# Performance work log

Hardware: AMD Instinct MI355X
Metric: run time of the kernel (lower is better)

## Reference

```python
import jax, jax.numpy as jnp
import numpy as np

BN_EPS = 1e-5


def maxpool2(x):
    # 2x2 max pool, stride 2: (B,C,H,W) -> (B,C,H//2,W//2)
    B, C, H, W = x.shape
    return x.reshape(B, C, H // 2, 2, W // 2, 2).max(axis=(3, 5))


def setup_inputs() -> dict:
    key = jax.random.key(0)
    ks = jax.random.split(key, 6)
    B, C, H, W = 4, 64, 96, 96   # in_dim = 64
    K, OD = 64, 64               # key_dim, out_dim
    sc = lambda fan: 1.0 / np.sqrt(fan)
    return {
        "c2": jax.random.normal(ks[0], (B, C, H, W), jnp.float32),
        "x": jax.random.normal(ks[1], (B, C, H, W), jnp.float32),
        # edge_att: Conv2d(2C->OD, 1x1, no bias) -> BN -> ReLU -> Conv2d(OD->1, 1x1) -> Sigmoid
        "w_ea1": jax.random.normal(ks[2], (OD, 2 * C), jnp.float32) * sc(2 * C),
        "bn_w": jnp.ones((OD,), jnp.float32),
        "bn_b": jnp.zeros((OD,), jnp.float32),
        "bn_m": jnp.zeros((OD,), jnp.float32),
        "bn_v": jnp.ones((OD,), jnp.float32),
        "w_ea2": jax.random.normal(ks[3], (1, OD), jnp.float32) * sc(OD),
        "b_ea2": jnp.zeros((1,), jnp.float32),
        # query_conv (shared for query AND key in the original forward)
        "w_q": jax.random.normal(ks[4], (K, C), jnp.float32) * sc(C),
        "b_q": jnp.zeros((K,), jnp.float32),
        "gamma": jnp.full((1,), 0.5, jnp.float32),
    }


def reference(c2, x, w_ea1, bn_w, bn_b, bn_m, bn_v, w_ea2, b_ea2, w_q, b_q, gamma):
    xp = maxpool2(x)        # (B,C,Hp,Wp)
    c2p = maxpool2(c2)
    B, C, H, W = x.shape
    Hp, Wp = xp.shape[2], xp.shape[3]

    # edge attention gate on pooled features -> (B,1,Hp,Wp)
    cat = jnp.concatenate([c2p, xp], axis=1)                       # (B,2C,Hp,Wp)
    h = jnp.einsum('oc,bchw->bohw', w_ea1, cat)
    bn_scale = (bn_w / jnp.sqrt(bn_v + BN_EPS))[None, :, None, None]
    h = jax.nn.relu((h - bn_m[None, :, None, None]) * bn_scale + bn_b[None, :, None, None])
    ea = jax.nn.sigmoid(jnp.einsum('oc,bchw->bohw', w_ea2, h) + b_ea2[None, :, None, None])

    # query at full res, key at pooled res (SAME conv weights, as in the source)
    q = jnp.einsum('kc,bchw->bkhw', w_q, x) + b_q[None, :, None, None]    # (B,K,H,W)
    k = jnp.einsum('kc,bchw->bkhw', w_q, xp) + b_q[None, :, None, None]   # (B,K,Hp,Wp)

    pq = q.reshape(B, -1, H * W)        # (B,K,N)
    pk = k.reshape(B, -1, Hp * Wp)      # (B,K,M)
    energy = jnp.einsum('bkn,bkm->bnm', pq, pk)                    # (B,N,M)
    attn = jax.nn.softmax(energy * ea.reshape(B, 1, Hp * Wp), axis=-1)

    v = xp.reshape(B, C, Hp * Wp)                                   # (B,C,M)
    out = jnp.einsum('bcm,bnm->bcn', v, attn).reshape(B, C, H, W)
    return gamma[0] * out + x
```

## Files before the change

kernel.cpp:

```cpp
#include <hip/hip_runtime.h>
#include <stdint.h>

#define B_ 4
#define C_ 64
#define H_ 96
#define W_ 96
#define HP_ 48
#define WP_ 48
#define N_ (H_*W_)
#define M_ (HP_*WP_)
#define KD_ 64
#define OD_ 64
#define BN_EPS 1e-5f
#define LOG2E 1.4426950408889634f
#define SHIFT2 28.853900817779268f
#define QT_ 48
#define QI_ (QT_/16)
#define QB_ (N_/QT_)
#define KVB_ 128
#define NT2_ (M_/KVB_)
#define KBUF_ 16384
#define BUF_ 32768
#define EAOFF_ 65536

typedef __bf16 bf16_t;
typedef bf16_t bf16x8 __attribute__((ext_vector_type(8)));
typedef bf16_t bf16x4 __attribute__((ext_vector_type(4)));
typedef float f32x4 __attribute__((ext_vector_type(4)));
typedef short short4v __attribute__((ext_vector_type(4)));
typedef short short8v __attribute__((ext_vector_type(8)));

static __device__ __forceinline__ unsigned short f2bf(float f) {
    unsigned int u = __builtin_bit_cast(unsigned int, f);
    u += 0x7fffu + ((u >> 16) & 1u);
    return (unsigned short)(u >> 16);
}

static __device__ __forceinline__ void gl_lds16(const unsigned short* g, unsigned short* l) {
#if __has_builtin(__builtin_amdgcn_global_load_lds)
    __builtin_amdgcn_global_load_lds(
        (const __attribute__((address_space(1))) unsigned int*)(const void*)g,
        (__attribute__((address_space(3))) unsigned int*)(void*)l, 16, 0, 0);
#endif
}

static __device__ __forceinline__ void setprio1() {
#if __has_builtin(__builtin_amdgcn_s_setprio)
    __builtin_amdgcn_s_setprio(1);
#endif
}
static __device__ __forceinline__ void setprio0() {
#if __has_builtin(__builtin_amdgcn_s_setprio)
    __builtin_amdgcn_s_setprio(0);
#endif
}
static __device__ __forceinline__ void schedbar0() {
#if __has_builtin(__builtin_amdgcn_sched_barrier)
    __builtin_amdgcn_sched_barrier(0);
#endif
}
static __device__ __forceinline__ void rawbar() {
#if __has_builtin(__builtin_amdgcn_s_barrier)
    __builtin_amdgcn_s_barrier();
#else
    __syncthreads();
#endif
}

__global__ __launch_bounds__(256) void prep_kernel(
    const float* __restrict__ x, const float* __restrict__ c2,
    const float* __restrict__ wq, const float* __restrict__ bq,
    const float* __restrict__ w1, const float* __restrict__ bnw, const float* __restrict__ bnb,
    const float* __restrict__ bnm, const float* __restrict__ bnv,
    const float* __restrict__ w2, const float* __restrict__ b2,
    unsigned short* __restrict__ kb, unsigned short* __restrict__ vb, float* __restrict__ ea) {

    __shared__ float lw1[OD_*2*C_];
    __shared__ float lwq[KD_*C_];
    __shared__ float xs[C_*33];
    __shared__ float c2s[C_*33];
    __shared__ float red[8][32];

    int tid = threadIdx.x;
    int b = blockIdx.x / 72;
    int m0 = (blockIdx.x % 72) * 32;

    for (int i = tid; i < OD_*2*C_; i += 256) lw1[i] = w1[i];
    for (int i = tid; i < KD_*C_; i += 256) lwq[i] = wq[i];
    for (int j = tid; j < 2048; j += 256) {
        int c = j >> 5, p = j & 31;
        int m = m0 + p;
        int hp = m / WP_, wp = m % WP_;
        size_t base = ((size_t)(b*C_ + c)*H_ + 2*hp)*W_ + 2*wp;
        const float* px = x + base;
        float mx = fmaxf(fmaxf(px[0], px[1]), fmaxf(px[W_], px[W_+1]));
        xs[c*33 + p] = mx;
        vb[(size_t)(b*C_ + c)*M_ + m] = f2bf(mx);
        const float* pc = c2 + base;
        c2s[c*33 + p] = fmaxf(fmaxf(pc[0], pc[1]), fmaxf(pc[W_], pc[W_+1]));
    }
    __syncthreads();

    int ml = tid & 31, oz = tid >> 5;
    int m = m0 + ml;

    float h[8] = {0,0,0,0,0,0,0,0};
    for (int c = 0; c < C_; c += 4) {
        float x0 = xs[c*33+ml], x1 = xs[(c+1)*33+ml], x2 = xs[(c+2)*33+ml], x3 = xs[(c+3)*33+ml];
        #pragma unroll
        for (int oi = 0; oi < 8; oi++) {
            const float4 wv = *(const float4*)&lwq[(oz*8 + oi)*C_ + c];
            h[oi] = fmaf(wv.x, x0, fmaf(wv.y, x1, fmaf(wv.z, x2, fmaf(wv.w, x3, h[oi]))));
        }
    }
    unsigned short tmp[8];
    #pragma unroll
    for (int oi = 0; oi < 8; oi++) tmp[oi] = f2bf(h[oi] + bq[oz*8 + oi]);
    *(uint4*)&kb[((size_t)b*M_ + m)*KD_ + oz*8] = *(const uint4*)tmp;

    float g[8] = {0,0,0,0,0,0,0,0};
    for (int c = 0; c < 2*C_; c += 4) {
        const float* srcb = (c < C_) ? &c2s[c*33] : &xs[(c - C_)*33];
        float x0 = srcb[ml], x1 = srcb[33+ml], x2 = srcb[66+ml], x3 = srcb[99+ml];
        #pragma unroll
        for (int oi = 0; oi < 8; oi++) {
            const float4 wv = *(const float4*)&lw1[(oz*8 + oi)*(2*C_) + c];
            g[oi] = fmaf(wv.x, x0, fmaf(wv.y, x1, fmaf(wv.z, x2, fmaf(wv.w, x3, g[oi]))));
        }
    }
    float z = 0.f;
    #pragma unroll
    for (int oi = 0; oi < 8; oi++) {
        int o = oz*8 + oi;
        float sc = bnw[o] * rsqrtf(bnv[o] + BN_EPS);
        float t = (g[oi] - bnm[o]) * sc + bnb[o];
        z += w2[o] * fmaxf(t, 0.f);
    }
    red[oz][ml] = z;
    __syncthreads();
    if (oz == 0) {
        float s = b2[0];
        #pragma unroll
        for (int i = 0; i < 8; i++) s += red[i][ml];
        ea[(size_t)b*M_ + m] = LOG2E / (1.f + __builtin_amdgcn_exp2f(-s * LOG2E));
    }
}

__global__ __launch_bounds__(256, 2) void attn_kernel(
    const float* __restrict__ wq, const float* __restrict__ bq,
    const unsigned short* __restrict__ kb, const unsigned short* __restrict__ vb,
    const float* __restrict__ ea, const float* __restrict__ x,
    const float* __restrict__ gamma_p, float* __restrict__ out) {

    __shared__ __align__(16) char smem[74752];

    int tid = threadIdx.x;
    int wave = tid >> 6, lane = tid & 63, quad = lane >> 4, l16 = lane & 15;
    int blk = blockIdx.x;
    int b = (blk & 7) >> 1;
    int n_base = ((blk & 1) * (QB_/2) + (blk >> 3)) * QT_;
    int xsw = l16 & 7;

    unsigned short* qlds = (unsigned short*)(smem + EAOFF_);
    {
        const float* xb = x + (size_t)b*C_*N_ + n_base;
        bf16x8 wh0, wh1, wl0, wl1;
        {
            float w8[8];
            unsigned short hs[8], ls[8];
            const float* wp0 = wq + (size_t)(wave*16 + l16)*C_ + quad*8;
            *(float4*)&w8[0] = *(const float4*)wp0;
            *(float4*)&w8[4] = *(const float4*)(wp0 + 4);
            #pragma unroll
            for (int j = 0; j < 8; j++) {
                hs[j] = f2bf(w8[j]);
                float hf = __builtin_bit_cast(float, (unsigned int)hs[j] << 16);
                ls[j] = f2bf(w8[j] - hf);
            }
            wh0 = __builtin_bit_cast(bf16x8, *(const uint4*)hs);
            wl0 = __builtin_bit_cast(bf16x8, *(const uint4*)ls);
            const float* wp1 = wp0 + 32;
            *(float4*)&w8[0] = *(const float4*)wp1;
            *(float4*)&w8[4] = *(const float4*)(wp1 + 4);
            #pragma unroll
            for (int j = 0; j < 8; j++) {
                hs[j] = f2bf(w8[j]);
                float hf = __builtin_bit_cast(float, (unsigned int)hs[j] << 16);
                ls[j] = f2bf(w8[j] - hf);
            }
            wh1 = __builtin_bit_cast(bf16x8, *(const uint4*)hs);
            wl1 = __builtin_bit_cast(bf16x8, *(const uint4*)ls);
        }
        float4 bq4 = *(const float4*)(bq + wave*16 + quad*4);

        f32x4 qacc[3];
        #pragma unroll
        for (int t = 0; t < 3; t++) qacc[t] = (f32x4){0.f,0.f,0.f,0.f};

        #pragma unroll
        for (int t = 0; t < 3; t++) {
            #pragma unroll
            for (int h = 0; h < 2; h++) {
                float v8[8];
                #pragma unroll
                for (int j = 0; j < 8; j++)
                    v8[j] = xb[(size_t)(h*32 + quad*8 + j)*N_ + t*16 + l16];
                unsigned short hs[8], ls[8];
                #pragma unroll
                for (int j = 0; j < 8; j++) {
                    hs[j] = f2bf(v8[j]);
                    float hf = __builtin_bit_cast(float, (unsigned int)hs[j] << 16);
                    ls[j] = f2bf(v8[j] - hf);
                }
                bf16x8 xh = __builtin_bit_cast(bf16x8, *(const uint4*)hs);
                bf16x8 xl = __builtin_bit_cast(bf16x8, *(const uint4*)ls);
                bf16x8 wh = h ? wh1 : wh0;
                bf16x8 wl = h ? wl1 : wl0;
#if __has_builtin(__builtin_amdgcn_mfma_f32_16x16x32_bf16)
                qacc[t] = __builtin_amdgcn_mfma_f32_16x16x32_bf16(wh, xh, qacc[t], 0, 0, 0);
                qacc[t] = __builtin_amdgcn_mfma_f32_16x16x32_bf16(wl, xh, qacc[t], 0, 0, 0);
                qacc[t] = __builtin_amdgcn_mfma_f32_16x16x32_bf16(wh, xl, qacc[t], 0, 0, 0);
#endif
            }
        }
        #pragma unroll
        for (int t = 0; t < 3; t++) {
            unsigned short q4[4];
            q4[0] = f2bf(qacc[t][0] + bq4.x);
            q4[1] = f2bf(qacc[t][1] + bq4.y);
            q4[2] = f2bf(qacc[t][2] + bq4.z);
            q4[3] = f2bf(qacc[t][3] + bq4.w);
            int n_abs = t*16 + l16;
            int kc = wave*2 + (quad >> 1);
            *(uint2*)&qlds[n_abs*64 + ((kc ^ (n_abs & 7)) << 3) + (quad & 1)*4] =
                *(const uint2*)q4;
        }
    }
    asm volatile("s_waitcnt lgkmcnt(0)" ::: "memory");
    __syncthreads();

    bf16x8 qf[QI_][2];
    #pragma unroll
    for (int qi = 0; qi < QI_; qi++) {
        const unsigned short* qp = qlds + (qi*16 + l16)*64;
        qf[qi][0] = __builtin_bit_cast(bf16x8, *(const uint4*)(qp + ((quad     ^ xsw) << 3)));
        qf[qi][1] = __builtin_bit_cast(bf16x8, *(const uint4*)(qp + (((quad+4) ^ xsw) << 3)));
    }
    asm volatile("s_waitcnt lgkmcnt(0)" ::: "memory");
    __syncthreads();

    f32x4 o2[QI_][4];
    f32x4 lacc[QI_];
    #pragma unroll
    for (int qi = 0; qi < QI_; qi++) {
        lacc[qi] = (f32x4){0.f,0.f,0.f,0.f};
        #pragma unroll
        for (int ct = 0; ct < 4; ct++) o2[qi][ct] = (f32x4){0.f,0.f,0.f,0.f};
    }
    const unsigned short ones_u[8] = {0x3F80,0x3F80,0x3F80,0x3F80,0x3F80,0x3F80,0x3F80,0x3F80};
    bf16x8 ones8 = __builtin_bit_cast(bf16x8, *(const uint4*)ones_u);

    const unsigned short* kbB = kb + (size_t)b*M_*KD_;
    const unsigned short* vbB = vb + (size_t)b*C_*M_;
    const float* eaB = ea + (size_t)b*M_;

    int r8  = tid >> 3;
    int mloc = (((r8 & 15) >> 2) << 3) + ((r8 >> 4) << 2) + (r8 & 3);
    int kcs = ((tid & 7) ^ (r8 & 7)) << 3;
    int c16 = tid >> 4;
    int vcs = ((tid & 15) ^ (c16 & 7)) << 3;

    auto STAGE = [&](int mb, char* buf) {
        unsigned short* kd = (unsigned short*)buf;
        unsigned short* vd = (unsigned short*)(buf + KBUF_);
        gl_lds16(kbB + (size_t)(mb +  0 + mloc)*KD_ + kcs, kd + 0*2048 + tid*8);
        gl_lds16(kbB + (size_t)(mb + 32 + mloc)*KD_ + kcs, kd + 1*2048 + tid*8);
        gl_lds16(kbB + (size_t)(mb + 64 + mloc)*KD_ + kcs, kd + 2*2048 + tid*8);
        gl_lds16(kbB + (size_t)(mb + 96 + mloc)*KD_ + kcs, kd + 3*2048 + tid*8);
        gl_lds16(vbB + (size_t)( 0 + c16)*M_ + mb + vcs, vd + 0*2048 + tid*8);
        gl_lds16(vbB + (size_t)(16 + c16)*M_ + mb + vcs, vd + 1*2048 + tid*8);
        gl_lds16(vbB + (size_t)(32 + c16)*M_ + mb + vcs, vd + 2*2048 + tid*8);
        gl_lds16(vbB + (size_t)(48 + c16)*M_ + mb + vcs, vd + 3*2048 + tid*8);
    };

    {
        const f32x4* eaV = (const f32x4*)eaB;
        f32x4* eaL = (f32x4*)(smem + EAOFF_);
        for (int i = tid; i < M_/4; i += 256) eaL[i] = eaV[i];
    }
    asm volatile("s_waitcnt lgkmcnt(0)" ::: "memory");
    __syncthreads();
    STAGE(0,    smem);
    STAGE(128,  smem + BUF_);
    asm volatile("s_waitcnt vmcnt(8)" ::: "memory");
    rawbar();
    asm volatile("" ::: "memory");

    const float* lds_ea = (const float*)(smem + EAOFF_);

    int kOffA0 = (wave*32 + l16)*64 + ((quad       ^ xsw) << 3);
    int kOffA1 = (wave*32 + l16)*64 + (((quad + 4) ^ xsw) << 3);
    int kOffB0 = kOffA0 + 16*64;
    int kOffB1 = kOffA1 + 16*64;
    int vch    = ((wave*4 + quad) ^ xsw) << 3;
    int eaIdx  = wave*32 + quad*8;

    struct FragSet {
        bf16x8 kfA0, kfA1, kfB0, kfB1;
        bf16x8 va0, va1, va2, va3;
        f32x4 eA, eB;
    };
    FragSet fA, fB;

    {
        unsigned short* kc = (unsigned short*)smem;
        unsigned short* vc = (unsigned short*)(smem + KBUF_);
        fA.eA  = *(const f32x4*)&lds_ea[0*KVB_ + eaIdx];
        fA.eB  = *(const f32x4*)&lds_ea[0*KVB_ + eaIdx + 4];
        fA.kfA0 = __builtin_bit_cast(bf16x8, *(const uint4*)(kc + kOffA0));
        fA.kfA1 = __builtin_bit_cast(bf16x8, *(const uint4*)(kc + kOffA1));
        fA.kfB0 = __builtin_bit_cast(bf16x8, *(const uint4*)(kc + kOffB0));
        fA.kfB1 = __builtin_bit_cast(bf16x8, *(const uint4*)(kc + kOffB1));
        fA.va0 = __builtin_bit_cast(bf16x8, *(const uint4*)(vc + (0*16 + l16)*KVB_ + vch));
        fA.va1 = __builtin_bit_cast(bf16x8, *(const uint4*)(vc + (1*16 + l16)*KVB_ + vch));
        fA.va2 = __builtin_bit_cast(bf16x8, *(const uint4*)(vc + (2*16 + l16)*KVB_ + vch));
        fA.va3 = __builtin_bit_cast(bf16x8, *(const uint4*)(vc + (3*16 + l16)*KVB_ + vch));
    }

#define ATTN_STEP(T_, CUR, NXT)                                                        \
    {                                                                                  \
        const int t_ = (T_);                                                           \
        if (t_ < NT2_ - 1) {                                                           \
            asm volatile("s_waitcnt vmcnt(0)" ::: "memory");   \
            schedbar0();                                                               \
            rawbar();                    \
            asm volatile("" ::: "memory");                                             \
            schedbar0();                                                               \
            if (t_ + 2 < NT2_) { STAGE((t_ + 2)*KVB_, smem + (t_ & 1)*BUF_); }         \
            unsigned short* kc_ = (unsigned short*)(smem + ((t_ + 1) & 1)*BUF_);       \
            unsigned short* vc_ = (unsigned short*)(smem + ((t_ + 1) & 1)*BUF_ + KBUF_); \
            NXT.eA  = *(const f32x4*)&lds_ea[(t_ + 1)*KVB_ + eaIdx];                   \
            NXT.eB  = *(const f32x4*)&lds_ea[(t_ + 1)*KVB_ + eaIdx + 4];               \
            NXT.kfA0 = __builtin_bit_cast(bf16x8, *(const uint4*)(kc_ + kOffA0));      \
            NXT.kfA1 = __builtin_bit_cast(bf16x8, *(const uint4*)(kc_ + kOffA1));      \
            NXT.kfB0 = __builtin_bit_cast(bf16x8, *(const uint4*)(kc_ + kOffB0));      \
            NXT.kfB1 = __builtin_bit_cast(bf16x8, *(const uint4*)(kc_ + kOffB1));      \
            NXT.va0 = __builtin_bit_cast(bf16x8, *(const uint4*)(vc_ + (0*16 + l16)*KVB_ + vch)); \
            NXT.va1 = __builtin_bit_cast(bf16x8, *(const uint4*)(vc_ + (1*16 + l16)*KVB_ + vch)); \
            NXT.va2 = __builtin_bit_cast(bf16x8, *(const uint4*)(vc_ + (2*16 + l16)*KVB_ + vch)); \
            NXT.va3 = __builtin_bit_cast(bf16x8, *(const uint4*)(vc_ + (3*16 + l16)*KVB_ + vch)); \
            schedbar0();                                                               \
            asm volatile("s_waitcnt lgkmcnt(10)" ::: "memory");  \
            schedbar0();                                                               \
        } else {                                                                       \
            schedbar0();                                                               \
            asm volatile("s_waitcnt lgkmcnt(0)" ::: "memory");      \
            schedbar0();                                                               \
        }                                                                              \
                               \
        f32x4 stA[QI_], stB[QI_];                                                      \
        setprio1();                                                                    \
        _Pragma("unroll")                                                              \
        for (int qi = 0; qi < QI_; qi++) {                                             \
            f32x4 zA = (f32x4){0.f,0.f,0.f,0.f};                                       \
            zA = __builtin_amdgcn_mfma_f32_16x16x32_bf16(CUR.kfA0, qf[qi][0], zA, 0, 0, 0); \
            zA = __builtin_amdgcn_mfma_f32_16x16x32_bf16(CUR.kfA1, qf[qi][1], zA, 0, 0, 0); \
            stA[qi] = zA;                                                              \
            f32x4 zB = (f32x4){0.f,0.f,0.f,0.f};                                       \
            zB = __builtin_amdgcn_mfma_f32_16x16x32_bf16(CUR.kfB0, qf[qi][0], zB, 0, 0, 0); \
            zB = __builtin_amdgcn_mfma_f32_16x16x32_bf16(CUR.kfB1, qf[qi][1], zB, 0, 0, 0); \
            stB[qi] = zB;                                                              \
        }                                                                              \
        setprio0();                                                                    \
        bf16x8 pk[QI_];                                                                \
        _Pragma("unroll")                                                              \
        for (int qi = 0; qi < QI_; qi++) {                                             \
            f32x4 pA, pB;                                                              \
            pA[0] = __builtin_amdgcn_exp2f(fmaf(stA[qi][0], CUR.eA[0], -SHIFT2));      \
            pA[1] = __builtin_amdgcn_exp2f(fmaf(stA[qi][1], CUR.eA[1], -SHIFT2));      \
            pA[2] = __builtin_amdgcn_exp2f(fmaf(stA[qi][2], CUR.eA[2], -SHIFT2));      \
            pA[3] = __builtin_amdgcn_exp2f(fmaf(stA[qi][3], CUR.eA[3], -SHIFT2));      \
            pB[0] = __builtin_amdgcn_exp2f(fmaf(stB[qi][0], CUR.eB[0], -SHIFT2));      \
            pB[1] = __builtin_amdgcn_exp2f(fmaf(stB[qi][1], CUR.eB[1], -SHIFT2));      \
            pB[2] = __builtin_amdgcn_exp2f(fmaf(stB[qi][2], CUR.eB[2], -SHIFT2));      \
            pB[3] = __builtin_amdgcn_exp2f(fmaf(stB[qi][3], CUR.eB[3], -SHIFT2));      \
            short4v pa = __builtin_bit_cast(short4v, __builtin_convertvector(pA, bf16x4)); \
            short4v pb = __builtin_bit_cast(short4v, __builtin_convertvector(pB, bf16x4)); \
            short8v p8 = __builtin_shufflevector(pa, pb, 0, 1, 2, 3, 4, 5, 6, 7);      \
            pk[qi] = __builtin_bit_cast(bf16x8, p8);                                   \
        }                                                                              \
        setprio1();                                                                    \
        _Pragma("unroll")                                                              \
        for (int qi = 0; qi < QI_; qi++) {                                             \
            o2[qi][0] = __builtin_amdgcn_mfma_f32_16x16x32_bf16(CUR.va0, pk[qi], o2[qi][0], 0, 0, 0); \
            o2[qi][1] = __builtin_amdgcn_mfma_f32_16x16x32_bf16(CUR.va1, pk[qi], o2[qi][1], 0, 0, 0); \
            o2[qi][2] = __builtin_amdgcn_mfma_f32_16x16x32_bf16(CUR.va2, pk[qi], o2[qi][2], 0, 0, 0); \
            o2[qi][3] = __builtin_amdgcn_mfma_f32_16x16x32_bf16(CUR.va3, pk[qi], o2[qi][3], 0, 0, 0); \
            lacc[qi]  = __builtin_amdgcn_mfma_f32_16x16x32_bf16(ones8,   pk[qi], lacc[qi], 0, 0, 0); \
        }                                                                              \
        setprio0();                                                                    \
    }

    for (int t = 0; t < NT2_; t += 2) {
        ATTN_STEP(t,     fA, fB);
        ATTN_STEP(t + 1, fB, fA);
    }
#undef ATTN_STEP

    __syncthreads();

    float* o_red0 = (float*)smem;
    float* o_red1 = o_red0 + QT_*68;
    float* l_red  = o_red1 + QT_*68;

    if (lane < 16) {
        #pragma unroll
        for (int qi = 0; qi < QI_; qi++) l_red[wave*QT_ + qi*16 + l16] = lacc[qi][0];
    }
    if (wave < 2) {
        float* od = (wave == 0) ? o_red0 : o_red1;
        #pragma unroll
        for (int qi = 0; qi < QI_; qi++)
            #pragma unroll
            for (int ct = 0; ct < 4; ct++)
                *(f32x4*)&od[(qi*16 + l16)*68 + ct*16 + quad*4] = o2[qi][ct];
    }
    __syncthreads();
    if (wave >= 2) {
        float* od = (wave == 2) ? o_red0 : o_red1;
        #pragma unroll
        for (int qi = 0; qi < QI_; qi++)
            #pragma unroll
            for (int ct = 0; ct < 4; ct++) {
                f32x4* p = (f32x4*)&od[(qi*16 + l16)*68 + ct*16 + quad*4];
                *p += o2[qi][ct];
            }
    }
    __syncthreads();
    if (tid < QT_) {
        float s = (l_red[tid] + l_red[QT_ + tid]) + (l_red[2*QT_ + tid] + l_red[3*QT_ + tid]);
        l_red[tid] = 1.f / s;
    }
    __syncthreads();

    float gmm = gamma_p[0];
    int c = tid >> 2, q4 = tid & 3;
    const float* xrow = x + ((size_t)b*C_ + c)*N_ + n_base;
    float* orow = out + ((size_t)b*C_ + c)*N_ + n_base;
    #pragma unroll
    for (int i = 0; i < QI_; i++) {
        int q0 = q4*4 + i*16;
        float4 xv = *(const float4*)(xrow + q0);
        float4 ov;
        float v0 = (o_red0[(q0+0)*68 + c] + o_red1[(q0+0)*68 + c]) * l_red[q0+0];
        float v1 = (o_red0[(q0+1)*68 + c] + o_red1[(q0+1)*68 + c]) * l_red[q0+1];
        float v2 = (o_red0[(q0+2)*68 + c] + o_red1[(q0+2)*68 + c]) * l_red[q0+2];
        float v3 = (o_red0[(q0+3)*68 + c] + o_red1[(q0+3)*68 + c]) * l_red[q0+3];
        ov.x = fmaf(gmm, v0, xv.x);
        ov.y = fmaf(gmm, v1, xv.y);
        ov.z = fmaf(gmm, v2, xv.z);
        ov.w = fmaf(gmm, v3, xv.w);
        *(float4*)(orow + q0) = ov;
    }
}

extern "C" void kernel_launch(void* const* d_in, const int* in_sizes, int n_in,
                              void* d_out, int out_size, void* d_ws, size_t ws_size,
                              hipStream_t stream) {
    const float* c2    = (const float*)d_in[0];
    const float* x     = (const float*)d_in[1];
    const float* w_ea1 = (const float*)d_in[2];
    const float* bn_w  = (const float*)d_in[3];
    const float* bn_b  = (const float*)d_in[4];
    const float* bn_m  = (const float*)d_in[5];
    const float* bn_v  = (const float*)d_in[6];
    const float* w_ea2 = (const float*)d_in[7];
    const float* b_ea2 = (const float*)d_in[8];
    const float* w_q   = (const float*)d_in[9];
    const float* b_q   = (const float*)d_in[10];
    const float* gamma = (const float*)d_in[11];
    float* out = (float*)d_out;

    char* ws = (char*)d_ws;
    float* ea            = (float*)(ws + 0);
    unsigned short* kb   = (unsigned short*)(ws + 36864);
    unsigned short* vb   = (unsigned short*)(ws + 1216512);

    prep_kernel<<<dim3((B_*M_)/32), dim3(256), 0, stream>>>(x, c2, w_q, b_q,
        w_ea1, bn_w, bn_b, bn_m, bn_v, w_ea2, b_ea2, kb, vb, ea);
    attn_kernel<<<dim3(B_*QB_), dim3(256), 0, stream>>>(w_q, b_q, kb, vb, ea, x, gamma, out);
}
```

Measured before the change: 148.0 us.

## Software-pipeline QK^T scores one tile ahead of softmax and PV

Moves the QK^T MFMA computation for the next KV tile to the end of the current step, so the exp2/softmax of tile t runs on scores computed in the previous iteration. Scores are double-buffered in registers (sX/sY), and a prologue computes the first tile's scores. The aim is to let VALU exp work overlap with MFMA work and hide LDS fragment-load latency. It raises register pressure and drops the partial lgkmcnt(10) wait in favour of a full lgkmcnt(0) before the next-tile MFMAs.

```diff
diff --git a/kernel.cpp b/kernel.cpp
--- a/kernel.cpp
+++ b/kernel.cpp
@@ -310,7 +310,9 @@
         bf16x8 va0, va1, va2, va3;
         f32x4 eA, eB;
     };
+    struct StSet { f32x4 sA[QI_]; f32x4 sB[QI_]; };
     FragSet fA, fB;
+    StSet sX, sY;
 
     {
         unsigned short* kc = (unsigned short*)smem;
@@ -326,8 +328,21 @@
         fA.va2 = __builtin_bit_cast(bf16x8, *(const uint4*)(vc + (2*16 + l16)*KVB_ + vch));
         fA.va3 = __builtin_bit_cast(bf16x8, *(const uint4*)(vc + (3*16 + l16)*KVB_ + vch));
     }
-
-#define ATTN_STEP(T_, CUR, NXT)                                                        \
+    asm volatile("s_waitcnt lgkmcnt(0)" ::: "memory");
+    schedbar0();
+    #pragma unroll
+    for (int qi = 0; qi < QI_; qi++) {
+        f32x4 zA = (f32x4){0.f,0.f,0.f,0.f};
+        zA = __builtin_amdgcn_mfma_f32_16x16x32_bf16(fA.kfA0, qf[qi][0], zA, 0, 0, 0);
+        zA = __builtin_amdgcn_mfma_f32_16x16x32_bf16(fA.kfA1, qf[qi][1], zA, 0, 0, 0);
+        sX.sA[qi] = zA;
+        f32x4 zB = (f32x4){0.f,0.f,0.f,0.f};
+        zB = __builtin_amdgcn_mfma_f32_16x16x32_bf16(fA.kfB0, qf[qi][0], zB, 0, 0, 0);
+        zB = __builtin_amdgcn_mfma_f32_16x16x32_bf16(fA.kfB1, qf[qi][1], zB, 0, 0, 0);
+        sX.sB[qi] = zB;
+    }
+
+#define ATTN_STEP(T_, CUR, NXT, SCUR, SNXT)                                            \
     {                                                                                  \
         const int t_ = (T_);                                                           \
         if (t_ < NT2_ - 1) {                                                           \
@@ -350,40 +365,20 @@
             NXT.va2 = __builtin_bit_cast(bf16x8, *(const uint4*)(vc_ + (2*16 + l16)*KVB_ + vch)); \
             NXT.va3 = __builtin_bit_cast(bf16x8, *(const uint4*)(vc_ + (3*16 + l16)*KVB_ + vch)); \
             schedbar0();                                                               \
-            asm volatile("s_waitcnt lgkmcnt(10)" ::: "memory");  \
-            schedbar0();                                                               \
-        } else {                                                                       \
-            schedbar0();                                                               \
-            asm volatile("s_waitcnt lgkmcnt(0)" ::: "memory");      \
-            schedbar0();                                                               \
         }                                                                              \
-                               \
-        f32x4 stA[QI_], stB[QI_];                                                      \
-        setprio1();                                                                    \
-        _Pragma("unroll")                                                              \
-        for (int qi = 0; qi < QI_; qi++) {                                             \
-            f32x4 zA = (f32x4){0.f,0.f,0.f,0.f};                                       \
-            zA = __builtin_amdgcn_mfma_f32_16x16x32_bf16(CUR.kfA0, qf[qi][0], zA, 0, 0, 0); \
-            zA = __builtin_amdgcn_mfma_f32_16x16x32_bf16(CUR.kfA1, qf[qi][1], zA, 0, 0, 0); \
-            stA[qi] = zA;                                                              \
-            f32x4 zB = (f32x4){0.f,0.f,0.f,0.f};                                       \
-            zB = __builtin_amdgcn_mfma_f32_16x16x32_bf16(CUR.kfB0, qf[qi][0], zB, 0, 0, 0); \
-            zB = __builtin_amdgcn_mfma_f32_16x16x32_bf16(CUR.kfB1, qf[qi][1], zB, 0, 0, 0); \
-            stB[qi] = zB;                                                              \
-        }                                                                              \
-        setprio0();                                                                    \
+                      \
         bf16x8 pk[QI_];                                                                \
         _Pragma("unroll")                                                              \
         for (int qi = 0; qi < QI_; qi++) {                                             \
             f32x4 pA, pB;                                                              \
-            pA[0] = __builtin_amdgcn_exp2f(fmaf(stA[qi][0], CUR.eA[0], -SHIFT2));      \
-            pA[1] = __builtin_amdgcn_exp2f(fmaf(stA[qi][1], CUR.eA[1], -SHIFT2));      \
-            pA[2] = __builtin_amdgcn_exp2f(fmaf(stA[qi][2], CUR.eA[2], -SHIFT2));      \
-            pA[3] = __builtin_amdgcn_exp2f(fmaf(stA[qi][3], CUR.eA[3], -SHIFT2));      \
-            pB[0] = __builtin_amdgcn_exp2f(fmaf(stB[qi][0], CUR.eB[0], -SHIFT2));      \
-            pB[1] = __builtin_amdgcn_exp2f(fmaf(stB[qi][1], CUR.eB[1], -SHIFT2));      \
-            pB[2] = __builtin_amdgcn_exp2f(fmaf(stB[qi][2], CUR.eB[2], -SHIFT2));      \
-            pB[3] = __builtin_amdgcn_exp2f(fmaf(stB[qi][3], CUR.eB[3], -SHIFT2));      \
+            pA[0] = __builtin_amdgcn_exp2f(fmaf(SCUR.sA[qi][0], CUR.eA[0], -SHIFT2));  \
+            pA[1] = __builtin_amdgcn_exp2f(fmaf(SCUR.sA[qi][1], CUR.eA[1], -SHIFT2));  \
+            pA[2] = __builtin_amdgcn_exp2f(fmaf(SCUR.sA[qi][2], CUR.eA[2], -SHIFT2));  \
+            pA[3] = __builtin_amdgcn_exp2f(fmaf(SCUR.sA[qi][3], CUR.eA[3], -SHIFT2));  \
+            pB[0] = __builtin_amdgcn_exp2f(fmaf(SCUR.sB[qi][0], CUR.eB[0], -SHIFT2));  \
+            pB[1] = __builtin_amdgcn_exp2f(fmaf(SCUR.sB[qi][1], CUR.eB[1], -SHIFT2));  \
+            pB[2] = __builtin_amdgcn_exp2f(fmaf(SCUR.sB[qi][2], CUR.eB[2], -SHIFT2));  \
+            pB[3] = __builtin_amdgcn_exp2f(fmaf(SCUR.sB[qi][3], CUR.eB[3], -SHIFT2));  \
             short4v pa = __builtin_bit_cast(short4v, __builtin_convertvector(pA, bf16x4)); \
             short4v pb = __builtin_bit_cast(short4v, __builtin_convertvector(pB, bf16x4)); \
             short8v p8 = __builtin_shufflevector(pa, pb, 0, 1, 2, 3, 4, 5, 6, 7);      \
@@ -399,11 +394,29 @@
             lacc[qi]  = __builtin_amdgcn_mfma_f32_16x16x32_bf16(ones8,   pk[qi], lacc[qi], 0, 0, 0); \
         }                                                                              \
         setprio0();                                                                    \
+            \
+        if (t_ < NT2_ - 1) {                                                           \
+            asm volatile("s_waitcnt lgkmcnt(0)" ::: "memory");   \
+            schedbar0();                                \
+            setprio1();                                                                \
+            _Pragma("unroll")                                                          \
+            for (int qi = 0; qi < QI_; qi++) {                                         \
+                f32x4 zA = (f32x4){0.f,0.f,0.f,0.f};                                   \
+                zA = __builtin_amdgcn_mfma_f32_16x16x32_bf16(NXT.kfA0, qf[qi][0], zA, 0, 0, 0); \
+                zA = __builtin_amdgcn_mfma_f32_16x16x32_bf16(NXT.kfA1, qf[qi][1], zA, 0, 0, 0); \
+                SNXT.sA[qi] = zA;                                                      \
+                f32x4 zB = (f32x4){0.f,0.f,0.f,0.f};                                   \
+                zB = __builtin_amdgcn_mfma_f32_16x16x32_bf16(NXT.kfB0, qf[qi][0], zB, 0, 0, 0); \
+                zB = __builtin_amdgcn_mfma_f32_16x16x32_bf16(NXT.kfB1, qf[qi][1], zB, 0, 0, 0); \
+                SNXT.sB[qi] = zB;                                                      \
+            }                                                                          \
+            setprio0();                                                                \
+        }                                                                              \
     }
 
     for (int t = 0; t < NT2_; t += 2) {
-        ATTN_STEP(t,     fA, fB);
-        ATTN_STEP(t + 1, fB, fA);
+        ATTN_STEP(t,     fA, fB, sX, sY);
+        ATTN_STEP(t + 1, fB, fA, sY, sX);
     }
 #undef ATTN_STEP
 
```

Measured after the change: 149.6 us. No clear change (+1.1%).
